# Performance work log

Measured on AMD Instinct MI355X. Metric: run time of the kernel, lower is better.

## Reference

```python
import jax, jax.numpy as jnp
import numpy as np

N_NODES = 50000
N_EDGES = 800000
F_IN = 128
HEADS = 4
C_OUT = 32
NEG_SLOPE = 0.2
BN_EPS = 1e-5


def _add_self_loops(edge_index, edge_attr, n):
    # PyG fill_value='mean': self-loop attr = mean of incoming edge attrs per node (0 if none)
    src, dst = edge_index[0], edge_index[1]
    deg = jax.ops.segment_sum(jnp.ones_like(edge_attr[:, 0]), dst, num_segments=n)
    loop_attr = jax.ops.segment_sum(edge_attr, dst, num_segments=n) / jnp.maximum(deg, 1.0)[:, None]
    loop = jnp.arange(n)
    src2 = jnp.concatenate([src, loop])
    dst2 = jnp.concatenate([dst, loop])
    attr2 = jnp.concatenate([edge_attr, loop_attr], axis=0)
    return src2, dst2, attr2


def _segment_softmax(logits, seg, n):
    m = jax.ops.segment_max(logits, seg, num_segments=n)
    m = jnp.where(jnp.isfinite(m), m, 0.0)
    ex = jnp.exp(logits - m[seg])
    s = jax.ops.segment_sum(ex, seg, num_segments=n)
    return ex / s[seg]


def _gatv2(x, src, dst, eattr, Wl, bl, Wr, br, We, att, bias, n):
    # x: [n, F]; returns [n, HEADS*C_OUT]
    xl = (x @ Wl + bl).reshape(n, HEADS, C_OUT)
    xr = (x @ Wr + br).reshape(n, HEADS, C_OUT)
    ea = (eattr @ We).reshape(-1, HEADS, C_OUT)
    xlj = xl[src]                                   # [E, H, C] gather
    msg = jax.nn.leaky_relu(xlj + xr[dst] + ea, NEG_SLOPE)
    logits = jnp.einsum('ehc,hc->eh', msg, att)     # [E, H]
    alpha = _segment_softmax(logits, dst, n)
    out = jax.ops.segment_sum(xlj * alpha[..., None], dst, num_segments=n)
    return out.reshape(n, HEADS * C_OUT) + bias


def _batchnorm(x, gamma, beta):
    mu = x.mean(axis=0)
    var = x.var(axis=0)
    return gamma * (x - mu) * jax.lax.rsqrt(var + BN_EPS) + beta


def setup_inputs() -> dict:
    key = jax.random.key(0)
    ks = jax.random.split(key, 20)
    HC = HEADS * C_OUT
    s = 0.05
    inp = {
        'emb': jax.random.normal(ks[0], (N_NODES, F_IN), dtype=jnp.float32),
        'edge_index': jax.random.randint(ks[1], (2, N_EDGES), 0, N_NODES, dtype=jnp.int64),
        'edge_weight': jax.random.uniform(ks[2], (N_EDGES, 1), dtype=jnp.float32),
        'Wl1': jax.random.normal(ks[3], (F_IN, HC)) * s,
        'bl1': jnp.zeros((HC,), jnp.float32),
        'Wr1': jax.random.normal(ks[4], (F_IN, HC)) * s,
        'br1': jnp.zeros((HC,), jnp.float32),
        'We1': jax.random.normal(ks[5], (1, HC)) * s,
        'att1': jax.random.normal(ks[6], (HEADS, C_OUT)) * s,
        'bias1': jnp.zeros((HC,), jnp.float32),
        'gamma1': jnp.ones((HC,), jnp.float32),
        'beta1': jnp.zeros((HC,), jnp.float32),
        'Wl2': jax.random.normal(ks[7], (HC, HC)) * s,
        'bl2': jnp.zeros((HC,), jnp.float32),
        'Wr2': jax.random.normal(ks[8], (HC, HC)) * s,
        'br2': jnp.zeros((HC,), jnp.float32),
        'We2': jax.random.normal(ks[9], (1, HC)) * s,
        'att2': jax.random.normal(ks[10], (HEADS, C_OUT)) * s,
        'bias2': jnp.zeros((HC,), jnp.float32),
    }
    return inp


def reference(emb, edge_index, edge_weight, Wl1, bl1, Wr1, br1, We1, att1, bias1,
              gamma1, beta1, Wl2, bl2, Wr2, br2, We2, att2, bias2):
    n = emb.shape[0]
    src, dst, eattr = _add_self_loops(edge_index, edge_weight, n)
    h1 = _gatv2(emb, src, dst, eattr, Wl1, bl1, Wr1, br1, We1, att1, bias1, n)
    h1 = jax.nn.elu(_batchnorm(h1, gamma1, beta1))
    h2 = _gatv2(h1, src, dst, eattr, Wl2, bl2, Wr2, br2, We2, att2, bias2, n)
    # fusion: mean over [input_emb, h1, h2] along stacked axis
    return (emb + h1 + h2) / 3.0
```

## Files before the change

### kernel.cpp

```cpp
#include <hip/hip_runtime.h>
#include <hip/hip_bf16.h>
#include <math.h>

#define N_NODES 50000
#define N_EDGES 800000
#define HC 128
#define SLOT 64

#define BM 128
#define NBX ((N_NODES + BM - 1) / BM)
#define NB_WPREP 256
#define NB_BUCKET ((N_EDGES + 255) / 256)

typedef short bh8 __attribute__((ext_vector_type(8)));
typedef float f4 __attribute__((ext_vector_type(4)));

__device__ __forceinline__ unsigned int pk2(float a, float b) {
  return (unsigned int)__bfloat16_as_ushort(__float2bfloat16(a)) |
         ((unsigned int)__bfloat16_as_ushort(__float2bfloat16(b)) << 16);
}

__global__ void k_prep(const float* __restrict__ Wl1, const float* __restrict__ Wr1,
                       const float* __restrict__ Wl2, const float* __restrict__ Wr2,
                       unsigned short* __restrict__ WtAll,
                       const int* __restrict__ ei, const float* __restrict__ ew,
                       int* __restrict__ cursor, int2* __restrict__ slots) {
  int bid = blockIdx.x;
  if (bid < NB_WPREP) {
    int m = bid >> 6;
    const float* src = (m == 0) ? Wl1 : (m == 1) ? Wr1 : (m == 2) ? Wl2 : Wr2;
    int idx = (bid & 63) * 256 + threadIdx.x;
    int k = idx >> 7, n = idx & 127;
    WtAll[((size_t)m * HC + n) * HC + k] =
        __bfloat16_as_ushort(__float2bfloat16(src[k * HC + n]));
    return;
  }
  int e = (bid - NB_WPREP) * 256 + threadIdx.x;
  if (e >= N_EDGES) return;
  int s = ei[e];
  int d = ei[N_EDGES + e];
  float w = ew[e];
  int pos = atomicAdd(cursor + d, 1);
  if (pos < SLOT) {
    slots[(size_t)d * SLOT + pos] = make_int2(s, __float_as_int(w));
  }
}

template <int LAYER2>
__global__ __launch_bounds__(256) void k_gemm_mfma(
    const float* __restrict__ X, const unsigned short* __restrict__ Wt,
    const float* __restrict__ b0, const float* __restrict__ b1,
    unsigned short* __restrict__ Y0b, float* __restrict__ Y1,
    const float* __restrict__ chsum, const float* __restrict__ chsq,
    const float* __restrict__ gamma, const float* __restrict__ beta) {
  __shared__ __align__(16) unsigned short Xls[128 * 128];
  __shared__ __align__(16) unsigned short Wls[128 * 128];
  __shared__ float ssc[HC], ssh[HC];
  int tid = threadIdx.x;
  if (LAYER2) {
    if (tid < HC) {
      float mu = chsum[tid] * (1.f / N_NODES);
      float var = chsq[tid] * (1.f / N_NODES) - mu * mu;
      float sc = gamma[tid] * rsqrtf(var + 1e-5f);
      ssc[tid] = sc;
      ssh[tid] = beta[tid] - mu * sc;
    }
    __syncthreads();
  }
  int row0 = blockIdx.x * BM;
  {
    int r = tid >> 1;
    int ks = (tid & 1) * 64;
    int gr = row0 + r;
    const float* xp = X + (size_t)gr * HC + ks;
    int sw = r & 15;
#pragma unroll
    for (int i = 0; i < 4; ++i) {
      float f[16];
      if (gr < N_NODES) {
        *(float4*)&f[0] = *(const float4*)(xp + i * 16);
        *(float4*)&f[4] = *(const float4*)(xp + i * 16 + 4);
        *(float4*)&f[8] = *(const float4*)(xp + i * 16 + 8);
        *(float4*)&f[12] = *(const float4*)(xp + i * 16 + 12);
      } else {
#pragma unroll
        for (int j = 0; j < 16; ++j) f[j] = 0.f;
      }
      if (LAYER2) {
#pragma unroll
        for (int j = 0; j < 16; ++j) {
          float y = fmaf(f[j], ssc[ks + i * 16 + j], ssh[ks + i * 16 + j]);
          f[j] = (y > 0.f) ? y : (__expf(y) - 1.f);
        }
      }
      int kg = (ks >> 3) + i * 2;
      *(uint4*)&Xls[r * 128 + ((kg ^ sw) * 8)] =
          make_uint4(pk2(f[0], f[1]), pk2(f[2], f[3]), pk2(f[4], f[5]), pk2(f[6], f[7]));
      *(uint4*)&Xls[r * 128 + (((kg + 1) ^ sw) * 8)] =
          make_uint4(pk2(f[8], f[9]), pk2(f[10], f[11]), pk2(f[12], f[13]), pk2(f[14], f[15]));
    }
  }
  int lane = tid & 63;
  int wv = tid >> 6;
  int lrow = lane & 15;
  int lq = lane >> 4;
  int rbase = wv * 32;
#pragma unroll
  for (int half = 0; half < 2; ++half) {
    if (half) __syncthreads();
    {
      int n = tid >> 1;
      int ks = (tid & 1) * 64;
      const unsigned short* wp = Wt + half * (HC * HC) + n * HC + ks;
      int swn = n & 15;
#pragma unroll
      for (int g = 0; g < 8; ++g) {
        uint4 v = *(const uint4*)(wp + g * 8);
        int kg = (ks >> 3) + g;
        *(uint4*)&Wls[n * 128 + ((kg ^ swn) * 8)] = v;
      }
    }
    __syncthreads();
    f4 acc[2][8];
#pragma unroll
    for (int mt = 0; mt < 2; ++mt)
#pragma unroll
      for (int nt = 0; nt < 8; ++nt) acc[mt][nt] = (f4){0.f, 0.f, 0.f, 0.f};
#pragma unroll
    for (int kk = 0; kk < 4; ++kk) {
      int kg = kk * 4 + lq;
      bh8 a0 = *(const bh8*)&Xls[(rbase + lrow) * 128 + ((kg ^ lrow) * 8)];
      bh8 a1 = *(const bh8*)&Xls[(rbase + 16 + lrow) * 128 + ((kg ^ lrow) * 8)];
#pragma unroll
      for (int nt = 0; nt < 8; ++nt) {
        bh8 b = *(const bh8*)&Wls[(nt * 16 + lrow) * 128 + ((kg ^ lrow) * 8)];
        acc[0][nt] = __builtin_amdgcn_mfma_f32_16x16x32_bf16(a0, b, acc[0][nt], 0, 0, 0);
        acc[1][nt] = __builtin_amdgcn_mfma_f32_16x16x32_bf16(a1, b, acc[1][nt], 0, 0, 0);
      }
    }
    const float* bb = half ? b1 : b0;
    float bv[8];
#pragma unroll
    for (int nt = 0; nt < 8; ++nt) bv[nt] = bb[nt * 16 + lrow];
#pragma unroll
    for (int mt = 0; mt < 2; ++mt) {
#pragma unroll
      for (int rr = 0; rr < 4; ++rr) {
        int gr = row0 + rbase + mt * 16 + lq * 4 + rr;
        if (gr < N_NODES) {
          if (half == 0) {
#pragma unroll
            for (int nt = 0; nt < 8; ++nt)
              Y0b[(size_t)gr * HC + nt * 16 + lrow] =
                  __bfloat16_as_ushort(__float2bfloat16(acc[mt][nt][rr] + bv[nt]));
          } else {
#pragma unroll
            for (int nt = 0; nt < 8; ++nt)
              Y1[(size_t)gr * HC + nt * 16 + lrow] = acc[mt][nt][rr] + bv[nt];
          }
        }
      }
    }
  }
}

template <int FINAL>
__global__ __launch_bounds__(256) void k_gat(
    const unsigned short* __restrict__ xlb, const float* __restrict__ xr,
    const int* __restrict__ cursor, const int2* __restrict__ slots,
    const float* __restrict__ We, const float* __restrict__ att,
    const float* __restrict__ bias, float* __restrict__ out,
    const float* __restrict__ emb, const float* __restrict__ h1p,
    const float* __restrict__ chsum, const float* __restrict__ chsq,
    const float* __restrict__ gamma, const float* __restrict__ beta) {
  int g = threadIdx.x >> 5;
  int lane = threadIdx.x & 31;
  int n = blockIdx.x * 8 + g;
  int fi = n * 32 + lane;
  const uint2* xl4 = (const uint2*)xlb;
  float4 xr4 = ((const float4*)xr)[fi];
  float4 we4 = ((const float4*)We)[lane];
  float4 at4 = ((const float4*)att)[lane];
  int deg = min(cursor[n], SLOT);
  int base = n * SLOT;
  int deg32 = min(deg, 32);

  int evs = 0;
  float evw = 0.f;
  if (lane < deg32) {
    int2 ev = slots[base + lane];
    evs = ev.x;
    evw = __int_as_float(ev.y);
  }
  float wsum = evw;
#pragma unroll
  for (int m = 16; m >= 1; m >>= 1) wsum += __shfl_xor(wsum, m);

  float l = 0.f;
  float4 o = make_float4(0.f, 0.f, 0.f, 0.f);

  auto edge_body = [&](float w, uint2 gc, bool valid) {
    float4 xlj;
    xlj.x = __uint_as_float(gc.x << 16);
    xlj.y = __uint_as_float(gc.x & 0xffff0000u);
    xlj.z = __uint_as_float(gc.y << 16);
    xlj.w = __uint_as_float(gc.y & 0xffff0000u);
    float4 v;
    v.x = fmaf(w, we4.x, xlj.x + xr4.x);
    v.y = fmaf(w, we4.y, xlj.y + xr4.y);
    v.z = fmaf(w, we4.z, xlj.z + xr4.z);
    v.w = fmaf(w, we4.w, xlj.w + xr4.w);
    v.x = fmaxf(v.x, 0.2f * v.x);
    v.y = fmaxf(v.y, 0.2f * v.y);
    v.z = fmaxf(v.z, 0.2f * v.z);
    v.w = fmaxf(v.w, 0.2f * v.w);
    float p = v.x * at4.x + v.y * at4.y + v.z * at4.z + v.w * at4.w;
    p += __shfl_xor(p, 1);
    p += __shfl_xor(p, 2);
    p += __shfl_xor(p, 4);
    float e = valid ? __expf(p) : 0.f;
    l += e;
    o.x = fmaf(e, xlj.x, o.x);
    o.y = fmaf(e, xlj.y, o.y);
    o.z = fmaf(e, xlj.z, o.z);
    o.w = fmaf(e, xlj.w, o.w);
  };
  auto fetch = [&](int j, uint2& qq, float& ww) {
    int jc = min(j, deg32 - 1);
    int s = __shfl(evs, jc, 32);
    ww = __shfl(evw, jc, 32);
    qq = xl4[s * 32 + lane];
  };

  if (deg32 > 0) {
    uint2 q0, q1, q2, q3;
    float w0, w1, w2, w3;
    fetch(0, q0, w0);
    fetch(1, q1, w1);
    fetch(2, q2, w2);
    fetch(3, q3, w3);
    for (int b = 0; b < deg32; b += 4) {
      uint2 c0 = q0, c1 = q1, c2 = q2, c3 = q3;
      float x0 = w0, x1 = w1, x2 = w2, x3 = w3;
      fetch(b + 4, q0, w0);
      fetch(b + 5, q1, w1);
      fetch(b + 6, q2, w2);
      fetch(b + 7, q3, w3);
      edge_body(x0, c0, true);
      edge_body(x1, c1, b + 1 < deg32);
      edge_body(x2, c2, b + 2 < deg32);
      edge_body(x3, c3, b + 3 < deg32);
    }
  }
  if (deg > 32) {
    for (int j = base + 32; j < base + deg; ++j) {
      int2 e = slots[j];
      float w = __int_as_float(e.y);
      wsum += w;
      uint2 gc = xl4[e.x * 32 + lane];
      edge_body(w, gc, true);
    }
  }
  {
    float wself = (deg > 0) ? wsum / (float)deg : 0.f;
    edge_body(wself, xl4[n * 32 + lane], true);
  }

  float inv = 1.f / l;
  float4 b4 = ((const float4*)bias)[lane];
  float4 r;
  r.x = fmaf(o.x, inv, b4.x);
  r.y = fmaf(o.y, inv, b4.y);
  r.z = fmaf(o.z, inv, b4.z);
  r.w = fmaf(o.w, inv, b4.w);
  if (FINAL) {
    float4 e4 = ((const float4*)emb)[fi];
    float4 h4 = ((const float4*)h1p)[fi];
    float4 cs = ((const float4*)chsum)[lane];
    float4 cq = ((const float4*)chsq)[lane];
    float4 gm = ((const float4*)gamma)[lane];
    float4 bt = ((const float4*)beta)[lane];
    const float invN = 1.f / N_NODES;
    float4 sc4, sh4;
    {
      float mu = cs.x * invN, var = cq.x * invN - mu * mu;
      sc4.x = gm.x * rsqrtf(var + 1e-5f); sh4.x = bt.x - mu * sc4.x;
      mu = cs.y * invN; var = cq.y * invN - mu * mu;
      sc4.y = gm.y * rsqrtf(var + 1e-5f); sh4.y = bt.y - mu * sc4.y;
      mu = cs.z * invN; var = cq.z * invN - mu * mu;
      sc4.z = gm.z * rsqrtf(var + 1e-5f); sh4.z = bt.z - mu * sc4.z;
      mu = cs.w * invN; var = cq.w * invN - mu * mu;
      sc4.w = gm.w * rsqrtf(var + 1e-5f); sh4.w = bt.w - mu * sc4.w;
    }
    float4 h;
    h.x = fmaf(h4.x, sc4.x, sh4.x);
    h.y = fmaf(h4.y, sc4.y, sh4.y);
    h.z = fmaf(h4.z, sc4.z, sh4.z);
    h.w = fmaf(h4.w, sc4.w, sh4.w);
    h.x = (h.x > 0.f) ? h.x : (__expf(h.x) - 1.f);
    h.y = (h.y > 0.f) ? h.y : (__expf(h.y) - 1.f);
    h.z = (h.z > 0.f) ? h.z : (__expf(h.z) - 1.f);
    h.w = (h.w > 0.f) ? h.w : (__expf(h.w) - 1.f);
    const float k3 = 1.f / 3.f;
    r.x = (e4.x + h.x + r.x) * k3;
    r.y = (e4.y + h.y + r.y) * k3;
    r.z = (e4.z + h.z + r.z) * k3;
    r.w = (e4.w + h.w + r.w) * k3;
  }
  ((float4*)out)[fi] = r;
}

#define BN_ROWS 200
__global__ __launch_bounds__(256) void k_bnstats(const float* __restrict__ h1,
                                                 float* __restrict__ chsum,
                                                 float* __restrict__ chsq) {
  int c = threadIdx.x & 127;
  int g = threadIdx.x >> 7;
  int r0 = blockIdx.x * BN_ROWS;
  float s = 0.f, q = 0.f;
  for (int r = r0 + g; r < r0 + BN_ROWS; r += 2) {
    float v = h1[(size_t)r * HC + c];
    s += v;
    q += v * v;
  }
  __shared__ float sh[256], shq[256];
  sh[threadIdx.x] = s;
  shq[threadIdx.x] = q;
  __syncthreads();
  if (g == 0) {
    atomicAdd(chsum + c, s + sh[threadIdx.x + 128]);
    atomicAdd(chsq + c, q + shq[threadIdx.x + 128]);
  }
}

extern "C" void kernel_launch(void* const* d_in, const int* in_sizes, int n_in,
                              void* d_out, int out_size, void* d_ws, size_t ws_size,
                              hipStream_t stream) {
  const float* emb = (const float*)d_in[0];
  const int* ei = (const int*)d_in[1];
  const float* ew = (const float*)d_in[2];
  const float* Wl1 = (const float*)d_in[3];
  const float* bl1 = (const float*)d_in[4];
  const float* Wr1 = (const float*)d_in[5];
  const float* br1 = (const float*)d_in[6];
  const float* We1 = (const float*)d_in[7];
  const float* att1 = (const float*)d_in[8];
  const float* bias1 = (const float*)d_in[9];
  const float* gamma1 = (const float*)d_in[10];
  const float* beta1 = (const float*)d_in[11];
  const float* Wl2 = (const float*)d_in[12];
  const float* bl2 = (const float*)d_in[13];
  const float* Wr2 = (const float*)d_in[14];
  const float* br2 = (const float*)d_in[15];
  const float* We2 = (const float*)d_in[16];
  const float* att2 = (const float*)d_in[17];
  const float* bias2 = (const float*)d_in[18];
  float* out = (float*)d_out;

  char* wsb = (char*)d_ws;
  size_t off = 0;
  auto alloc = [&](size_t bytes) -> void* {
    void* p = (void*)(wsb + off);
    off += (bytes + 255) & ~(size_t)255;
    return p;
  };
  int* cursor = (int*)alloc((size_t)N_NODES * 4);
  float* chsum = (float*)alloc(HC * 4);
  float* chsq = (float*)alloc(HC * 4);
  size_t zero_bytes = off;
  unsigned short* WtAll = (unsigned short*)alloc((size_t)4 * HC * HC * 2);
  int2* slots = (int2*)alloc((size_t)N_NODES * SLOT * 8);
  unsigned short* xlb = (unsigned short*)alloc((size_t)N_NODES * HC * 2);
  float* xr = (float*)alloc((size_t)N_NODES * HC * 4);
  float* h1 = (float*)alloc((size_t)N_NODES * HC * 4);

  hipMemsetAsync(d_ws, 0, zero_bytes, stream);

  k_prep<<<NB_WPREP + NB_BUCKET, 256, 0, stream>>>(Wl1, Wr1, Wl2, Wr2, WtAll,
                                                   ei, ew, cursor, slots);
  k_gemm_mfma<0><<<NBX, 256, 0, stream>>>(emb, WtAll, bl1, br1, xlb, xr,
                                          nullptr, nullptr, nullptr, nullptr);
  k_gat<0><<<N_NODES / 8, 256, 0, stream>>>(xlb, xr, cursor, slots, We1, att1,
                                            bias1, h1, nullptr, nullptr, nullptr,
                                            nullptr, nullptr, nullptr);
  k_bnstats<<<N_NODES / BN_ROWS, 256, 0, stream>>>(h1, chsum, chsq);
  k_gemm_mfma<1><<<NBX, 256, 0, stream>>>(h1, WtAll + 2 * HC * HC, bl2, br2,
                                          xlb, xr, chsum, chsq, gamma1, beta1);
  k_gat<1><<<N_NODES / 8, 256, 0, stream>>>(xlb, xr, cursor, slots, We2, att2,
                                            bias2, out, emb, h1, chsum, chsq,
                                            gamma1, beta1);
}
```

Before: 308.0 us.

## Pack edge slots to 32 bits, fp8 layer-2 features, fuse prep launches

```diff
diff --git a/kernel.cpp b/kernel.cpp
--- a/kernel.cpp
+++ b/kernel.cpp
@@ -9,48 +9,38 @@
 
 #define BM 128
 #define NBX ((N_NODES + BM - 1) / BM)
-#define NB_WPREP 256
-#define NB_BUCKET ((N_EDGES + 255) / 256)
+#define NB_EDGE ((N_EDGES + 255) / 256)
 
 typedef short bh8 __attribute__((ext_vector_type(8)));
 typedef float f4 __attribute__((ext_vector_type(4)));
+typedef float f2 __attribute__((ext_vector_type(2)));
 
 __device__ __forceinline__ unsigned int pk2(float a, float b) {
   return (unsigned int)__bfloat16_as_ushort(__float2bfloat16(a)) |
          ((unsigned int)__bfloat16_as_ushort(__float2bfloat16(b)) << 16);
 }
 
-__global__ void k_prep(const float* __restrict__ Wl1, const float* __restrict__ Wr1,
-                       const float* __restrict__ Wl2, const float* __restrict__ Wr2,
-                       unsigned short* __restrict__ WtAll,
-                       const int* __restrict__ ei, const float* __restrict__ ew,
-                       int* __restrict__ cursor, int2* __restrict__ slots) {
-  int bid = blockIdx.x;
-  if (bid < NB_WPREP) {
-    int m = bid >> 6;
-    const float* src = (m == 0) ? Wl1 : (m == 1) ? Wr1 : (m == 2) ? Wl2 : Wr2;
-    int idx = (bid & 63) * 256 + threadIdx.x;
-    int k = idx >> 7, n = idx & 127;
-    WtAll[((size_t)m * HC + n) * HC + k] =
-        __bfloat16_as_ushort(__float2bfloat16(src[k * HC + n]));
-    return;
-  }
-  int e = (bid - NB_WPREP) * 256 + threadIdx.x;
-  if (e >= N_EDGES) return;
-  int s = ei[e];
-  int d = ei[N_EDGES + e];
-  float w = ew[e];
-  int pos = atomicAdd(cursor + d, 1);
-  if (pos < SLOT) {
-    slots[(size_t)d * SLOT + pos] = make_int2(s, __float_as_int(w));
-  }
-}
-
-template <int LAYER2>
-__global__ __launch_bounds__(256) void k_gemm_mfma(
-    const float* __restrict__ X, const unsigned short* __restrict__ Wt,
+__global__ __launch_bounds__(256) void k_wprep(
+    const float* __restrict__ Wl1, const float* __restrict__ Wr1,
+    const float* __restrict__ Wl2, const float* __restrict__ Wr2,
+    unsigned short* __restrict__ WtAll, int* __restrict__ cursor,
+    float* __restrict__ chsum, float* __restrict__ chsq) {
+  int gid = blockIdx.x * 256 + threadIdx.x;
+  int m = gid >> 14;
+  int idx = gid & 16383;
+  const float* src = (m == 0) ? Wl1 : (m == 1) ? Wr1 : (m == 2) ? Wl2 : Wr2;
+  int k = idx >> 7, n = idx & 127;
+  WtAll[((size_t)m * HC + n) * HC + k] =
+      __bfloat16_as_ushort(__float2bfloat16(src[k * HC + n]));
+  if (gid < N_NODES) cursor[gid] = 0;
+  if (gid < HC) { chsum[gid] = 0.f; chsq[gid] = 0.f; }
+}
+
+template <int LAYER2, int F8>
+__device__ __forceinline__ void gemm_tile(
+    int bx, const float* __restrict__ X, const unsigned short* __restrict__ Wt,
     const float* __restrict__ b0, const float* __restrict__ b1,
-    unsigned short* __restrict__ Y0b, float* __restrict__ Y1,
+    void* __restrict__ Y0, float* __restrict__ Y1,
     const float* __restrict__ chsum, const float* __restrict__ chsq,
     const float* __restrict__ gamma, const float* __restrict__ beta) {
   __shared__ __align__(16) unsigned short Xls[128 * 128];
@@ -67,7 +57,7 @@
     }
     __syncthreads();
   }
-  int row0 = blockIdx.x * BM;
+  int row0 = bx * BM;
   {
     int r = tid >> 1;
     int ks = (tid & 1) * 64;
@@ -149,10 +139,20 @@
         int gr = row0 + rbase + mt * 16 + lq * 4 + rr;
         if (gr < N_NODES) {
           if (half == 0) {
-#pragma unroll
-            for (int nt = 0; nt < 8; ++nt)
-              Y0b[(size_t)gr * HC + nt * 16 + lrow] =
-                  __bfloat16_as_ushort(__float2bfloat16(acc[mt][nt][rr] + bv[nt]));
+            if (F8) {
+#pragma unroll
+              for (int nt = 0; nt < 8; ++nt) {
+                float v = acc[mt][nt][rr] + bv[nt];
+                int p = __builtin_amdgcn_cvt_pk_fp8_f32(v, v, 0, false);
+                ((unsigned char*)Y0)[(size_t)gr * HC + nt * 16 + lrow] =
+                    (unsigned char)(p & 0xff);
+              }
+            } else {
+#pragma unroll
+              for (int nt = 0; nt < 8; ++nt)
+                ((unsigned short*)Y0)[(size_t)gr * HC + nt * 16 + lrow] =
+                    __bfloat16_as_ushort(__float2bfloat16(acc[mt][nt][rr] + bv[nt]));
+            }
           } else {
 #pragma unroll
             for (int nt = 0; nt < 8; ++nt)
@@ -164,10 +164,44 @@
   }
 }
 
-template <int FINAL>
+__global__ __launch_bounds__(256) void k_g1prep(
+    const float* __restrict__ X, const unsigned short* __restrict__ Wt,
+    const float* __restrict__ b0, const float* __restrict__ b1,
+    unsigned short* __restrict__ Y0b, float* __restrict__ Y1,
+    const int* __restrict__ ei, const float* __restrict__ ew,
+    int* __restrict__ cursor, unsigned int* __restrict__ slots) {
+  int bid = blockIdx.x;
+  if (bid < NBX) {
+    gemm_tile<0, 0>(bid, X, Wt, b0, b1, (void*)Y0b, Y1, nullptr, nullptr,
+                    nullptr, nullptr);
+    return;
+  }
+  int e = (bid - NBX) * 256 + threadIdx.x;
+  if (e >= N_EDGES) return;
+  int s = ei[e];
+  int d = ei[N_EDGES + e];
+  float w = ew[e];
+  unsigned int wq = min((unsigned int)(w * 65536.f + 0.5f), 65535u);
+  int pos = atomicAdd(cursor + d, 1);
+  if (pos < SLOT) {
+    slots[(size_t)d * SLOT + pos] = ((unsigned int)s << 16) | wq;
+  }
+}
+
+__global__ __launch_bounds__(256) void k_gemm2(
+    const float* __restrict__ X, const unsigned short* __restrict__ Wt,
+    const float* __restrict__ b0, const float* __restrict__ b1,
+    unsigned char* __restrict__ Y0f8, float* __restrict__ Y1,
+    const float* __restrict__ chsum, const float* __restrict__ chsq,
+    const float* __restrict__ gamma, const float* __restrict__ beta) {
+  gemm_tile<1, 1>(blockIdx.x, X, Wt, b0, b1, (void*)Y0f8, Y1, chsum, chsq,
+                  gamma, beta);
+}
+
+template <int FINAL, int F8>
 __global__ __launch_bounds__(256) void k_gat(
-    const unsigned short* __restrict__ xlb, const float* __restrict__ xr,
-    const int* __restrict__ cursor, const int2* __restrict__ slots,
+    const void* __restrict__ xlv, const float* __restrict__ xr,
+    const int* __restrict__ cursor, const unsigned int* __restrict__ slots,
     const float* __restrict__ We, const float* __restrict__ att,
     const float* __restrict__ bias, float* __restrict__ out,
     const float* __restrict__ emb, const float* __restrict__ h1p,
@@ -177,7 +211,8 @@
   int lane = threadIdx.x & 31;
   int n = blockIdx.x * 8 + g;
   int fi = n * 32 + lane;
-  const uint2* xl4 = (const uint2*)xlb;
+  const uint2* xl2 = (const uint2*)xlv;
+  const unsigned int* xf = (const unsigned int*)xlv;
   float4 xr4 = ((const float4*)xr)[fi];
   float4 we4 = ((const float4*)We)[lane];
   float4 at4 = ((const float4*)att)[lane];
@@ -185,13 +220,8 @@
   int base = n * SLOT;
   int deg32 = min(deg, 32);
 
-  int evs = 0;
-  float evw = 0.f;
-  if (lane < deg32) {
-    int2 ev = slots[base + lane];
-    evs = ev.x;
-    evw = __int_as_float(ev.y);
-  }
+  unsigned int ev = (lane < deg32) ? slots[base + lane] : 0u;
+  float evw = (float)(ev & 0xffffu) * (1.f / 65536.f);
   float wsum = evw;
 #pragma unroll
   for (int m = 16; m >= 1; m >>= 1) wsum += __shfl_xor(wsum, m);
@@ -199,12 +229,22 @@
   float l = 0.f;
   float4 o = make_float4(0.f, 0.f, 0.f, 0.f);
 
+  auto decode = [&](uint2 gc) -> float4 {
+    float4 xlj;
+    if (F8) {
+      f2 ab = __builtin_amdgcn_cvt_pk_f32_fp8((int)gc.x, false);
+      f2 cd = __builtin_amdgcn_cvt_pk_f32_fp8((int)gc.x, true);
+      xlj.x = ab[0]; xlj.y = ab[1]; xlj.z = cd[0]; xlj.w = cd[1];
+    } else {
+      xlj.x = __uint_as_float(gc.x << 16);
+      xlj.y = __uint_as_float(gc.x & 0xffff0000u);
+      xlj.z = __uint_as_float(gc.y << 16);
+      xlj.w = __uint_as_float(gc.y & 0xffff0000u);
+    }
+    return xlj;
+  };
   auto edge_body = [&](float w, uint2 gc, bool valid) {
-    float4 xlj;
-    xlj.x = __uint_as_float(gc.x << 16);
-    xlj.y = __uint_as_float(gc.x & 0xffff0000u);
-    xlj.z = __uint_as_float(gc.y << 16);
-    xlj.w = __uint_as_float(gc.y & 0xffff0000u);
+    float4 xlj = decode(gc);
     float4 v;
     v.x = fmaf(w, we4.x, xlj.x + xr4.x);
     v.y = fmaf(w, we4.y, xlj.y + xr4.y);
@@ -227,9 +267,11 @@
   };
   auto fetch = [&](int j, uint2& qq, float& ww) {
     int jc = min(j, deg32 - 1);
-    int s = __shfl(evs, jc, 32);
-    ww = __shfl(evw, jc, 32);
-    qq = xl4[s * 32 + lane];
+    unsigned int evj = __shfl(ev, jc, 32);
+    ww = (float)(evj & 0xffffu) * (1.f / 65536.f);
+    int s = (int)(evj >> 16);
+    if (F8) qq.x = xf[s * 32 + lane];
+    else qq = xl2[s * 32 + lane];
   };
 
   if (deg32 > 0) {
@@ -254,16 +296,22 @@
   }
   if (deg > 32) {
     for (int j = base + 32; j < base + deg; ++j) {
-      int2 e = slots[j];
-      float w = __int_as_float(e.y);
+      unsigned int evj = slots[j];
+      float w = (float)(evj & 0xffffu) * (1.f / 65536.f);
       wsum += w;
-      uint2 gc = xl4[e.x * 32 + lane];
+      int s = (int)(evj >> 16);
+      uint2 gc;
+      if (F8) gc.x = xf[s * 32 + lane];
+      else gc = xl2[s * 32 + lane];
       edge_body(w, gc, true);
     }
   }
   {
     float wself = (deg > 0) ? wsum / (float)deg : 0.f;
-    edge_body(wself, xl4[n * 32 + lane], true);
+    uint2 gs;
+    if (F8) gs.x = xf[n * 32 + lane];
+    else gs = xl2[n * 32 + lane];
+    edge_body(wself, gs, true);
   }
 
   float inv = 1.f / l;
@@ -367,26 +415,23 @@
   int* cursor = (int*)alloc((size_t)N_NODES * 4);
   float* chsum = (float*)alloc(HC * 4);
   float* chsq = (float*)alloc(HC * 4);
-  size_t zero_bytes = off;
   unsigned short* WtAll = (unsigned short*)alloc((size_t)4 * HC * HC * 2);
-  int2* slots = (int2*)alloc((size_t)N_NODES * SLOT * 8);
+  unsigned int* slots = (unsigned int*)alloc((size_t)N_NODES * SLOT * 4);
   unsigned short* xlb = (unsigned short*)alloc((size_t)N_NODES * HC * 2);
+  unsigned char* xlf8 = (unsigned char*)alloc((size_t)N_NODES * HC);
   float* xr = (float*)alloc((size_t)N_NODES * HC * 4);
   float* h1 = (float*)alloc((size_t)N_NODES * HC * 4);
 
-  hipMemsetAsync(d_ws, 0, zero_bytes, stream);
-
-  k_prep<<<NB_WPREP + NB_BUCKET, 256, 0, stream>>>(Wl1, Wr1, Wl2, Wr2, WtAll,
-                                                   ei, ew, cursor, slots);
-  k_gemm_mfma<0><<<NBX, 256, 0, stream>>>(emb, WtAll, bl1, br1, xlb, xr,
-                                          nullptr, nullptr, nullptr, nullptr);
-  k_gat<0><<<N_NODES / 8, 256, 0, stream>>>(xlb, xr, cursor, slots, We1, att1,
-                                            bias1, h1, nullptr, nullptr, nullptr,
-                                            nullptr, nullptr, nullptr);
+  k_wprep<<<256, 256, 0, stream>>>(Wl1, Wr1, Wl2, Wr2, WtAll, cursor, chsum, chsq);
+  k_g1prep<<<NBX + NB_EDGE, 256, 0, stream>>>(emb, WtAll, bl1, br1, xlb, xr,
+                                              ei, ew, cursor, slots);
+  k_gat<0, 0><<<N_NODES / 8, 256, 0, stream>>>(xlb, xr, cursor, slots, We1, att1,
+                                               bias1, h1, nullptr, nullptr,
+                                               nullptr, nullptr, nullptr, nullptr);
   k_bnstats<<<N_NODES / BN_ROWS, 256, 0, stream>>>(h1, chsum, chsq);
-  k_gemm_mfma<1><<<NBX, 256, 0, stream>>>(h1, WtAll + 2 * HC * HC, bl2, br2,
-                                          xlb, xr, chsum, chsq, gamma1, beta1);
-  k_gat<1><<<N_NODES / 8, 256, 0, stream>>>(xlb, xr, cursor, slots, We2, att2,
-                                            bias2, out, emb, h1, chsum, chsq,
-                                            gamma1, beta1);
-}
+  k_gemm2<<<NBX, 256, 0, stream>>>(h1, WtAll + 2 * HC * HC, bl2, br2, xlf8, xr,
+                                   chsum, chsq, gamma1, beta1);
+  k_gat<1, 1><<<N_NODES / 8, 256, 0, stream>>>(xlf8, xr, cursor, slots, We2, att2,
+                                               bias2, out, emb, h1, chsum, chsq,
+                                               gamma1, beta1);
+}
```

Result: faster. 295.2 us (-4.2%).
